# Optimization experiments

Measured on AMD Instinct MI355X. Metric: run time of the kernel, lower is better.

## Reference

```python
import jax, jax.numpy as jnp
import numpy as np

NV, NE, NI, D = 100000, 20000, 600000, 128

def setup_inputs() -> dict:
    key = jax.random.key(0)
    ks = jax.random.split(key, 16)
    inp = {
        'vfeat': jax.random.normal(ks[0], (NV, D), jnp.float32),
        'efeat': jax.random.normal(ks[1], (NE, D), jnp.float32),
        # positive regularization weights/sums (HNHN degree-based normalizers)
        'v_reg_weight': jax.random.uniform(ks[2], (NV, 1), jnp.float32, 0.5, 1.5),
        'v_reg_sum': jax.random.uniform(ks[3], (NV, 1), jnp.float32, 0.5, 1.5),
        'e_reg_weight': jax.random.uniform(ks[4], (NE, 1), jnp.float32, 0.5, 1.5),
        'e_reg_sum': jax.random.uniform(ks[5], (NE, 1), jnp.float32, 0.5, 1.5),
        'node_idx': jax.random.randint(ks[6], (NI,), 0, NV),
        'hedge_idx': jax.random.randint(ks[7], (NI,), 0, NE),
    }
    s = 1.0 / np.sqrt(D)
    inp['W1'] = jax.random.uniform(ks[8], (D, D), jnp.float32, -s, s)
    inp['b1'] = jax.random.uniform(ks[9], (D,), jnp.float32, -s, s)
    inp['Wve'] = jax.random.uniform(ks[10], (D, D), jnp.float32, -s, s)
    inp['bve'] = jax.random.uniform(ks[11], (D,), jnp.float32, -s, s)
    inp['Wev'] = jax.random.uniform(ks[12], (D, D), jnp.float32, -s, s)
    inp['bev'] = jax.random.uniform(ks[13], (D,), jnp.float32, -s, s)
    return inp


def reference(vfeat, efeat, v_reg_weight, v_reg_sum, e_reg_weight, e_reg_sum,
              node_idx, hedge_idx, W1, b1, Wve, bve, Wev, bev):
    # vertex projection (vtx_lin_1layer)
    feat_v = vfeat @ W1.T + b1                      # [NV, Dv]
    # node -> hyperedge pass ('in' etype)
    Wh_n = feat_v @ Wve.T + bve                     # [NV, De]
    w_in = v_reg_weight[node_idx] / e_reg_sum[hedge_idx]   # [NI, 1]
    feat_e = jax.ops.segment_sum(w_in * Wh_n[node_idx], hedge_idx,
                                 num_segments=NE)   # [NE, De]
    # hyperedge -> node pass ('con' etype)
    Wh_e = feat_e @ Wev.T + bev                     # [NE, Dv]
    w_con = e_reg_weight[hedge_idx] / v_reg_sum[node_idx]  # [NI, 1]
    feat_v_out = jax.ops.segment_sum(w_con * Wh_e[hedge_idx], node_idx,
                                     num_segments=NV)  # [NV, Dv]
    return feat_v_out
```

## Files before the change

kernel.cpp:

```cpp
#include <hip/hip_runtime.h>

#define D 128
#define PADE 16
#define PADV 4

typedef unsigned short ushort_t;
typedef short short8 __attribute__((ext_vector_type(8)));
typedef ushort_t ushort8v __attribute__((ext_vector_type(8)));
typedef float f32x4 __attribute__((ext_vector_type(4)));

static __device__ __forceinline__ unsigned short f2bf(float f){
  unsigned int b = __float_as_uint(f);
  unsigned int r = (b + 0x7FFFu + ((b >> 16) & 1u)) >> 16;
  return (unsigned short)r;
}
static __device__ __forceinline__ float bf2f(unsigned short u){
  return __uint_as_float(((unsigned int)u) << 16);
}


__global__ void k_u1(const float* __restrict__ W1, const float* __restrict__ Wve,
                     const float* __restrict__ b1, const float* __restrict__ bve,
                     float* __restrict__ Wcf, float* __restrict__ bc,
                     const float* __restrict__ vfeat, ushort_t* __restrict__ vbf, int nvd,
                     const int* __restrict__ node_idx, const int* __restrict__ hedge_idx, int ni,
                     int* __restrict__ cnt_e_pad, int* __restrict__ cnt_v_pad,
                     int* __restrict__ rank_e, int* __restrict__ rank_v,
                     int vb, int cb){
  int t = threadIdx.x;
  int i = blockIdx.x;
  if (i < 128){
    int r = i;
    if (t < D){
      float acc = 0.f;
      for (int k = 0; k < D; ++k) acc += Wve[r * D + k] * W1[k * D + t];
      Wcf[r * D + t] = acc;
      if (t == 0){
        float s = 0.f;
        for (int k = 0; k < D; ++k) s += Wve[r * D + k] * b1[k];
        bc[r] = s + bve[r];
      }
    }
    return;
  }
  int j = i - 128;
  int total = vb + cb;
  long a0 = (long)j * vb / total, a1 = (long)(j + 1) * vb / total;
  if (a1 != a0){
    size_t base = (size_t)a0 * 8192;
#pragma unroll
    for (int c = 0; c < 4; ++c){
      size_t e8 = base + (size_t)c * 2048 + (size_t)t * 8;
      if (e8 < (size_t)nvd){
        float4 v0 = *(const float4*)&vfeat[e8];
        float4 v1 = *(const float4*)&vfeat[e8 + 4];
        ushort8v h;
        h[0] = f2bf(v0.x); h[1] = f2bf(v0.y); h[2] = f2bf(v0.z); h[3] = f2bf(v0.w);
        h[4] = f2bf(v1.x); h[5] = f2bf(v1.y); h[6] = f2bf(v1.z); h[7] = f2bf(v1.w);
        *(ushort8v*)&vbf[e8] = h;
      }
    }
  } else {
    int idx = (int)(j - a0) * 256 + t;
    if (idx < ni){
      int n = node_idx[idx], h = hedge_idx[idx];
      rank_e[idx] = atomicAdd(&cnt_e_pad[h * PADE], 1);
      rank_v[idx] = atomicAdd(&cnt_v_pad[n * PADV], 1);
    }
  }
}


__device__ __forceinline__ void scan_partial_body(const int* cnt, int n, int stride,
                                                  int* bsum, int b){
  __shared__ int s[256];
  int t = threadIdx.x;
  int base = b * 1024;
  int acc = 0;
  for (int j = t; j < 1024; j += 256){
    int idx = base + j;
    if (idx < n) acc += cnt[(size_t)idx * stride];
  }
  s[t] = acc; __syncthreads();
  for (int o = 128; o > 0; o >>= 1){
    if (t < o) s[t] += s[t + o];
    __syncthreads();
  }
  if (t == 0) bsum[b] = s[0];
}

__global__ void k_scan_partial2(const int* __restrict__ ce, int ne, int* __restrict__ bse,
                                const int* __restrict__ cv, int nv, int* __restrict__ bsv,
                                int nbe){
  if ((int)blockIdx.x < nbe) scan_partial_body(ce, ne, PADE, bse, blockIdx.x);
  else                       scan_partial_body(cv, nv, PADV, bsv, blockIdx.x - nbe);
}

__device__ __forceinline__ void scan_final_body(const int* cnt, int n, int stride,
                                                const int* bsum, int nb,
                                                int* off, int* cout, int b){
  __shared__ int s[256];
  int t = threadIdx.x;
  int bv = (t < nb) ? bsum[t] : 0;
  s[t] = bv; __syncthreads();
  for (int o = 1; o < 256; o <<= 1){
    int x = (t >= o) ? s[t - o] : 0;
    __syncthreads();
    s[t] += x;
    __syncthreads();
  }
  int myb = (b == 0) ? 0 : s[b - 1];
  __syncthreads();

  int base = b * 1024 + t * 4;
  int v0 = (base + 0 < n) ? cnt[(size_t)(base + 0) * stride] : 0;
  int v1 = (base + 1 < n) ? cnt[(size_t)(base + 1) * stride] : 0;
  int v2 = (base + 2 < n) ? cnt[(size_t)(base + 2) * stride] : 0;
  int v3 = (base + 3 < n) ? cnt[(size_t)(base + 3) * stride] : 0;
  int lsum = v0 + v1 + v2 + v3;
  s[t] = lsum; __syncthreads();
  for (int o = 1; o < 256; o <<= 1){
    int x = (t >= o) ? s[t - o] : 0;
    __syncthreads();
    s[t] += x;
    __syncthreads();
  }
  int excl = s[t] - lsum + myb;
  if (base + 0 < n){ off[base + 0] = excl;                cout[base + 0] = v0; }
  if (base + 1 < n){ off[base + 1] = excl + v0;           cout[base + 1] = v1; }
  if (base + 2 < n){ off[base + 2] = excl + v0 + v1;      cout[base + 2] = v2; }
  if (base + 3 < n){ off[base + 3] = excl + v0 + v1 + v2; cout[base + 3] = v3; }
}

__global__ void k_scan_final2(const int* __restrict__ ce, int ne, const int* __restrict__ bse,
                              int* __restrict__ off_e, int* __restrict__ cnt_e,
                              const int* __restrict__ cv, int nv, const int* __restrict__ bsv,
                              int* __restrict__ off_v, int* __restrict__ cnt_v,
                              int nbe, int nbv){
  if ((int)blockIdx.x < nbe)
    scan_final_body(ce, ne, PADE, bse, nbe, off_e, cnt_e, blockIdx.x);
  else
    scan_final_body(cv, nv, PADV, bsv, nbv, off_v, cnt_v, blockIdx.x - nbe);
}


__global__ void k_u2(const float* __restrict__ Wev, const float* __restrict__ Wcf,
                     const float* __restrict__ bc,
                     ushort_t* __restrict__ Wcc, float* __restrict__ bvec1,
                     const int* __restrict__ node_idx, const int* __restrict__ hedge_idx,
                     const int* __restrict__ rank_e, int ni,
                     const int* __restrict__ off_e, int* __restrict__ elist_v){
  int t = threadIdx.x;
  int i = blockIdx.x;
  if (i < 128){
    int r = i;
    if (t < D){
      float acc = 0.f;
      for (int k = 0; k < D; ++k) acc += Wev[r * D + k] * Wcf[k * D + t];
      Wcc[r * D + t] = f2bf(acc);
      if (t == 0){
        float s = 0.f;
        for (int k = 0; k < D; ++k) s += Wev[r * D + k] * bc[k];
        bvec1[r] = s;
      }
    }
  } else {
    int idx = (i - 128) * 256 + t;
    if (idx < ni){
      int pe = off_e[hedge_idx[idx]] + rank_e[idx];
      elist_v[pe] = node_idx[idx];
    }
  }
}


__global__ void k_u3(const ushort_t* __restrict__ vbf,
                     const int* __restrict__ off_e, const int* __restrict__ cnt_e,
                     const int* __restrict__ elist,
                     const float* __restrict__ vrw, const float* __restrict__ ers,
                     float* __restrict__ agg, float* __restrict__ wsum,
                     int ne, int sb, int total,
                     const int* __restrict__ node_idx, const int* __restrict__ hedge_idx,
                     const int* __restrict__ rank_v, int ni,
                     const int* __restrict__ off_v, int* __restrict__ vlist_e){
  int i = blockIdx.x;
  long a0 = (long)i * sb / total, a1 = (long)(i + 1) * sb / total;
  if (a1 != a0){
    int tid = threadIdx.x;
    int seg = (int)a0 * 16 + (tid >> 4);
    if (seg >= ne) return;
    int l16 = tid & 15;
    int s = off_e[seg], n = cnt_e[seg];
    float inv = 1.0f / ers[seg];

    float acc[8];
#pragma unroll
    for (int c = 0; c < 8; ++c) acc[c] = 0.f;
    float wa = 0.f;

    int j = 0;
    for (; j + 2 <= n; j += 2){
      int r0 = elist[s + j];
      int r1 = elist[s + j + 1];
      float w0 = vrw[r0];
      float w1 = vrw[r1];
      ushort8v x0 = *(const ushort8v*)&vbf[(size_t)r0 * D + l16 * 8];
      ushort8v x1 = *(const ushort8v*)&vbf[(size_t)r1 * D + l16 * 8];
      wa += w0 + w1;
#pragma unroll
      for (int c = 0; c < 8; ++c) acc[c] += w0 * bf2f(x0[c]) + w1 * bf2f(x1[c]);
    }
    if (j < n){
      int r0 = elist[s + j];
      float w0 = vrw[r0];
      ushort8v x0 = *(const ushort8v*)&vbf[(size_t)r0 * D + l16 * 8];
      wa += w0;
#pragma unroll
      for (int c = 0; c < 8; ++c) acc[c] += w0 * bf2f(x0[c]);
    }

    float* dp = &agg[(size_t)seg * D + l16 * 8];
    float4 o0, o1;
    o0.x = acc[0] * inv; o0.y = acc[1] * inv; o0.z = acc[2] * inv; o0.w = acc[3] * inv;
    o1.x = acc[4] * inv; o1.y = acc[5] * inv; o1.z = acc[6] * inv; o1.w = acc[7] * inv;
    *(float4*)dp = o0;
    *(float4*)(dp + 4) = o1;
    if (l16 == 0) wsum[seg] = wa * inv;
  } else {
    int idx = (int)(i - a0) * 256 + threadIdx.x;
    if (idx < ni){
      int pv = off_v[node_idx[idx]] + rank_v[idx];
      vlist_e[pv] = hedge_idx[idx];
    }
  }
}


__global__ __launch_bounds__(256, 2)
void k_gemm_rs(const float* __restrict__ A, const ushort_t* __restrict__ Wb,
               const float* __restrict__ wsum, const float* __restrict__ bvec1,
               const float* __restrict__ bev, ushort_t* __restrict__ out, int M){
  __shared__ ushort_t Al[64 * D];

  const int t = threadIdx.x;
  const int w = t >> 6;
  const int l = t & 63;
  const int l15 = l & 15;
  const int lh = l >> 4;

  short8 breg[4][8];
#pragma unroll
  for (int kc = 0; kc < 4; ++kc)
#pragma unroll
    for (int n0 = 0; n0 < 8; ++n0)
      breg[kc][n0] = *(const short8*)&Wb[(n0 * 16 + l15) * D + kc * 32 + lh * 8];

  float bv1_r[8], bev_r[8];
#pragma unroll
  for (int n0 = 0; n0 < 8; ++n0){
    bv1_r[n0] = bvec1[n0 * 16 + l15];
    bev_r[n0] = bev[n0 * 16 + l15];
  }

  const int r_st = t >> 2;
  const int q_st = t & 3;
  const int ntile = (M + 63) >> 6;

  for (int tile = blockIdx.x; tile < ntile; tile += gridDim.x){
    const int row0 = tile << 6;
    __syncthreads();
    {
      int r = row0 + r_st;
      ushort8v h[4];
      if (r < M){
        const float4* src = (const float4*)&A[(size_t)r * D + q_st * 32];
        float4 v[8];
#pragma unroll
        for (int ii = 0; ii < 8; ++ii) v[ii] = src[ii];
#pragma unroll
        for (int c = 0; c < 4; ++c){
          h[c][0] = f2bf(v[2*c].x);   h[c][1] = f2bf(v[2*c].y);
          h[c][2] = f2bf(v[2*c].z);   h[c][3] = f2bf(v[2*c].w);
          h[c][4] = f2bf(v[2*c+1].x); h[c][5] = f2bf(v[2*c+1].y);
          h[c][6] = f2bf(v[2*c+1].z); h[c][7] = f2bf(v[2*c+1].w);
        }
      } else {
#pragma unroll
        for (int c = 0; c < 4; ++c) h[c] = (ushort8v){0,0,0,0,0,0,0,0};
      }
#pragma unroll
      for (int c = 0; c < 4; ++c){
        int col = q_st * 32 + c * 8;
        int swz = col ^ ((r_st & 7) << 3);
        *(ushort8v*)&Al[r_st * D + swz] = h[c];
      }
    }
    __syncthreads();

    f32x4 acc[8];
#pragma unroll
    for (int n0 = 0; n0 < 8; ++n0) acc[n0] = (f32x4){0.f, 0.f, 0.f, 0.f};

#pragma unroll
    for (int kc = 0; kc < 4; ++kc){
      const int arow = w * 16 + l15;
      const int acol = (kc * 32 + lh * 8) ^ ((l15 & 7) << 3);
      short8 a = *(const short8*)&Al[arow * D + acol];
#pragma unroll
      for (int n0 = 0; n0 < 8; ++n0)
        acc[n0] = __builtin_amdgcn_mfma_f32_16x16x32_bf16(a, breg[kc][n0], acc[n0], 0, 0, 0);
    }

    const int rbase = row0 + w * 16 + lh * 4;
    float w4[4];
#pragma unroll
    for (int rg = 0; rg < 4; ++rg)
      w4[rg] = (rbase + rg < M) ? wsum[rbase + rg] : 0.f;
#pragma unroll
    for (int n0 = 0; n0 < 8; ++n0){
      const int colo = n0 * 16 + l15;
#pragma unroll
      for (int rg = 0; rg < 4; ++rg){
        int row = rbase + rg;
        if (row < M)
          out[(size_t)row * D + colo] = f2bf(acc[n0][rg] + w4[rg] * bv1_r[n0] + bev_r[n0]);
      }
    }
  }
}


__global__ void k_scatter2(const ushort_t* __restrict__ src,
                           const int* __restrict__ off, const int* __restrict__ cnt,
                           const int* __restrict__ list,
                           const float* __restrict__ wnum, const float* __restrict__ dsum,
                           float* __restrict__ dst, int nseg){
  int tid = threadIdx.x;
  int seg = blockIdx.x * 16 + (tid >> 4);
  if (seg >= nseg) return;
  int l16 = tid & 15;
  int s = off[seg], n = cnt[seg];
  float inv = 1.0f / dsum[seg];

  float acc[8];
#pragma unroll
  for (int c = 0; c < 8; ++c) acc[c] = 0.f;

  int j = 0;
  for (; j + 2 <= n; j += 2){
    int r0 = list[s + j];
    int r1 = list[s + j + 1];
    float w0 = wnum[r0] * inv;
    float w1 = wnum[r1] * inv;
    ushort8v x0 = *(const ushort8v*)&src[(size_t)r0 * D + l16 * 8];
    ushort8v x1 = *(const ushort8v*)&src[(size_t)r1 * D + l16 * 8];
#pragma unroll
    for (int c = 0; c < 8; ++c) acc[c] += w0 * bf2f(x0[c]) + w1 * bf2f(x1[c]);
  }
  if (j < n){
    int r0 = list[s + j];
    float w0 = wnum[r0] * inv;
    ushort8v x0 = *(const ushort8v*)&src[(size_t)r0 * D + l16 * 8];
#pragma unroll
    for (int c = 0; c < 8; ++c) acc[c] += w0 * bf2f(x0[c]);
  }

  float* dp = &dst[(size_t)seg * D + l16 * 8];
  float4 o0, o1;
  o0.x = acc[0]; o0.y = acc[1]; o0.z = acc[2]; o0.w = acc[3];
  o1.x = acc[4]; o1.y = acc[5]; o1.z = acc[6]; o1.w = acc[7];
  *(float4*)dp = o0;
  *(float4*)(dp + 4) = o1;
}


static inline int cdiv(int a, int b){ return (a + b - 1) / b; }

extern "C" void kernel_launch(void* const* d_in, const int* in_sizes, int n_in,
                              void* d_out, int out_size, void* d_ws, size_t ws_size,
                              hipStream_t stream){
  const float* vfeat        = (const float*)d_in[0];
  const float* v_reg_weight = (const float*)d_in[2];
  const float* v_reg_sum    = (const float*)d_in[3];
  const float* e_reg_weight = (const float*)d_in[4];
  const float* e_reg_sum    = (const float*)d_in[5];
  const int*   node_idx     = (const int*)d_in[6];
  const int*   hedge_idx    = (const int*)d_in[7];
  const float* W1  = (const float*)d_in[8];
  const float* b1  = (const float*)d_in[9];
  const float* Wve = (const float*)d_in[10];
  const float* bve = (const float*)d_in[11];
  const float* Wev = (const float*)d_in[12];
  const float* bev = (const float*)d_in[13];

  const int NV = in_sizes[2];
  const int NE = in_sizes[4];
  const int NI = in_sizes[6];
  const int NVD = NV * D;

  char* p = (char*)d_ws;
  auto alloc = [&](size_t nbytes) -> void* {
    void* q = (void*)p;
    p += (nbytes + 255) & ~(size_t)255;
    return q;
  };

  char* zstart = p;
  int* cnt_e_pad = (int*)alloc((size_t)NE * PADE * 4);
  int* cnt_v_pad = (int*)alloc((size_t)NV * PADV * 4);
  size_t zbytes = (size_t)(p - zstart);

  int* cnt_e  = (int*)alloc((size_t)NE * 4);
  int* cnt_v  = (int*)alloc((size_t)NV * 4);
  int* off_e  = (int*)alloc((size_t)NE * 4);
  int* off_v  = (int*)alloc((size_t)NV * 4);
  int* bsum_e = (int*)alloc(1024 * 4);
  int* bsum_v = (int*)alloc(1024 * 4);
  int* rank_e = (int*)alloc((size_t)NI * 4);
  int* rank_v = (int*)alloc((size_t)NI * 4);
  int* elist_v = (int*)alloc((size_t)NI * 4);
  int* vlist_e = (int*)alloc((size_t)NI * 4);
  float* Wcf     = (float*)alloc((size_t)D * D * 4);
  float* bc      = (float*)alloc((size_t)D * 4);
  ushort_t* Wcc  = (ushort_t*)alloc((size_t)D * D * 2);
  float* bvec1   = (float*)alloc((size_t)D * 4);
  ushort_t* Wh_e = (ushort_t*)alloc((size_t)NE * D * 2);

  ushort_t* vbf  = (ushort_t*)d_out;
  float*    agg  = (float*)((char*)d_out + (size_t)NVD * 2);
  float*    wsum = (float*)((char*)d_out + (size_t)NVD * 2 + (size_t)NE * D * 4);

  hipMemsetAsync(zstart, 0, zbytes, stream);

  int cb = cdiv(NI, 256);
  int vb = cdiv(NVD, 8192);
  k_u1<<<128 + vb + cb, 256, 0, stream>>>(W1, Wve, b1, bve, Wcf, bc,
                                          vfeat, vbf, NVD,
                                          node_idx, hedge_idx, NI,
                                          cnt_e_pad, cnt_v_pad, rank_e, rank_v,
                                          vb, cb);

  int nbe = cdiv(NE, 1024), nbv = cdiv(NV, 1024);
  k_scan_partial2<<<nbe + nbv, 256, 0, stream>>>(cnt_e_pad, NE, bsum_e,
                                                 cnt_v_pad, NV, bsum_v, nbe);
  k_scan_final2<<<nbe + nbv, 256, 0, stream>>>(cnt_e_pad, NE, bsum_e, off_e, cnt_e,
                                               cnt_v_pad, NV, bsum_v, off_v, cnt_v,
                                               nbe, nbv);

  k_u2<<<128 + cb, 256, 0, stream>>>(Wev, Wcf, bc, Wcc, bvec1,
                                     node_idx, hedge_idx, rank_e, NI,
                                     off_e, elist_v);

  int sb = cdiv(NE, 16);
  int u3_total = sb + cb;
  k_u3<<<u3_total, 256, 0, stream>>>(vbf, off_e, cnt_e, elist_v,
                                     v_reg_weight, e_reg_sum,
                                     agg, wsum, NE, sb, u3_total,
                                     node_idx, hedge_idx, rank_v, NI,
                                     off_v, vlist_e);

  k_gemm_rs<<<cdiv(NE, 64), 256, 0, stream>>>(agg, Wcc, wsum, bvec1, bev, Wh_e, NE);

  k_scatter2<<<cdiv(NV, 16), 256, 0, stream>>>(Wh_e, off_v, cnt_v, vlist_e,
                                               e_reg_weight, v_reg_sum,
                                               (float*)d_out, NV);
}
```

Before: 166.0 us.

## Fuse hyperedge gather-aggregation with the Wev GEMM via shared memory

The hyperedge aggregation kernel now accumulates 64 hyperedges per block into a padded shared-memory tile and runs the bf16 MFMA projection directly from it, writing Wh_e. This removes the fp32 agg/wsum round trip through global memory and one kernel launch. In exchange each block does four times as many segments serially in the gather phase, holds about 34KB of LDS, and carries extra register pressure from the preloaded weight fragments, which can reduce occupancy and latency hiding for the irregular gathers.

```diff
diff --git a/kernel.cpp b/kernel.cpp
--- a/kernel.cpp
+++ b/kernel.cpp
@@ -3,6 +3,7 @@
 #define D 128
 #define PADE 16
 #define PADV 4
+#define AGLD 132
 
 typedef unsigned short ushort_t;
 typedef short short8 __attribute__((ext_vector_type(8)));
@@ -174,75 +175,79 @@
 }
 
 
-__global__ void k_u3(const ushort_t* __restrict__ vbf,
-                     const int* __restrict__ off_e, const int* __restrict__ cnt_e,
-                     const int* __restrict__ elist,
-                     const float* __restrict__ vrw, const float* __restrict__ ers,
-                     float* __restrict__ agg, float* __restrict__ wsum,
-                     int ne, int sb, int total,
-                     const int* __restrict__ node_idx, const int* __restrict__ hedge_idx,
-                     const int* __restrict__ rank_v, int ni,
-                     const int* __restrict__ off_v, int* __restrict__ vlist_e){
+__global__ __launch_bounds__(256, 2)
+void k_u3f(const ushort_t* __restrict__ vbf,
+           const int* __restrict__ off_e, const int* __restrict__ cnt_e,
+           const int* __restrict__ elist,
+           const float* __restrict__ vrw, const float* __restrict__ ers,
+           const ushort_t* __restrict__ Wcc, const float* __restrict__ bvec1,
+           const float* __restrict__ bev, ushort_t* __restrict__ Wh_e,
+           int ne, int sbf, int total,
+           const int* __restrict__ node_idx, const int* __restrict__ hedge_idx,
+           const int* __restrict__ rank_v, int ni,
+           const int* __restrict__ off_v, int* __restrict__ vlist_e){
+  __shared__ float aggl[64 * AGLD];
+  __shared__ float wsl[64];
+
   int i = blockIdx.x;
-  long a0 = (long)i * sb / total, a1 = (long)(i + 1) * sb / total;
-  if (a1 != a0){
-    int tid = threadIdx.x;
-    int seg = (int)a0 * 16 + (tid >> 4);
-    if (seg >= ne) return;
-    int l16 = tid & 15;
-    int s = off_e[seg], n = cnt_e[seg];
-    float inv = 1.0f / ers[seg];
-
-    float acc[8];
-#pragma unroll
-    for (int c = 0; c < 8; ++c) acc[c] = 0.f;
-    float wa = 0.f;
-
-    int j = 0;
-    for (; j + 2 <= n; j += 2){
-      int r0 = elist[s + j];
-      int r1 = elist[s + j + 1];
-      float w0 = vrw[r0];
-      float w1 = vrw[r1];
-      ushort8v x0 = *(const ushort8v*)&vbf[(size_t)r0 * D + l16 * 8];
-      ushort8v x1 = *(const ushort8v*)&vbf[(size_t)r1 * D + l16 * 8];
-      wa += w0 + w1;
-#pragma unroll
-      for (int c = 0; c < 8; ++c) acc[c] += w0 * bf2f(x0[c]) + w1 * bf2f(x1[c]);
-    }
-    if (j < n){
-      int r0 = elist[s + j];
-      float w0 = vrw[r0];
-      ushort8v x0 = *(const ushort8v*)&vbf[(size_t)r0 * D + l16 * 8];
-      wa += w0;
-#pragma unroll
-      for (int c = 0; c < 8; ++c) acc[c] += w0 * bf2f(x0[c]);
-    }
-
-    float* dp = &agg[(size_t)seg * D + l16 * 8];
-    float4 o0, o1;
-    o0.x = acc[0] * inv; o0.y = acc[1] * inv; o0.z = acc[2] * inv; o0.w = acc[3] * inv;
-    o1.x = acc[4] * inv; o1.y = acc[5] * inv; o1.z = acc[6] * inv; o1.w = acc[7] * inv;
-    *(float4*)dp = o0;
-    *(float4*)(dp + 4) = o1;
-    if (l16 == 0) wsum[seg] = wa * inv;
-  } else {
+  long a0 = (long)i * sbf / total, a1 = (long)(i + 1) * sbf / total;
+  if (a1 == a0){
     int idx = (int)(i - a0) * 256 + threadIdx.x;
     if (idx < ni){
       int pv = off_v[node_idx[idx]] + rank_v[idx];
       vlist_e[pv] = hedge_idx[idx];
     }
-  }
-}
-
-
-__global__ __launch_bounds__(256, 2)
-void k_gemm_rs(const float* __restrict__ A, const ushort_t* __restrict__ Wb,
-               const float* __restrict__ wsum, const float* __restrict__ bvec1,
-               const float* __restrict__ bev, ushort_t* __restrict__ out, int M){
-  __shared__ ushort_t Al[64 * D];
-
+    return;
+  }
+
+  const int blk = (int)a0;
   const int t = threadIdx.x;
+
+  {
+    int gid = t >> 4, l16 = t & 15;
+#pragma unroll
+    for (int it = 0; it < 4; ++it){
+      int row = it * 16 + gid;
+      int seg = blk * 64 + row;
+      float acc[8];
+#pragma unroll
+      for (int c = 0; c < 8; ++c) acc[c] = 0.f;
+      float wa = 0.f, inv = 0.f;
+      if (seg < ne){
+        int s = off_e[seg], n = cnt_e[seg];
+        inv = 1.0f / ers[seg];
+        int j = 0;
+        for (; j + 2 <= n; j += 2){
+          int r0 = elist[s + j];
+          int r1 = elist[s + j + 1];
+          float w0 = vrw[r0];
+          float w1 = vrw[r1];
+          ushort8v x0 = *(const ushort8v*)&vbf[(size_t)r0 * D + l16 * 8];
+          ushort8v x1 = *(const ushort8v*)&vbf[(size_t)r1 * D + l16 * 8];
+          wa += w0 + w1;
+#pragma unroll
+          for (int c = 0; c < 8; ++c) acc[c] += w0 * bf2f(x0[c]) + w1 * bf2f(x1[c]);
+        }
+        if (j < n){
+          int r0 = elist[s + j];
+          float w0 = vrw[r0];
+          ushort8v x0 = *(const ushort8v*)&vbf[(size_t)r0 * D + l16 * 8];
+          wa += w0;
+#pragma unroll
+          for (int c = 0; c < 8; ++c) acc[c] += w0 * bf2f(x0[c]);
+        }
+      }
+      float* ap = &aggl[row * AGLD + l16 * 8];
+      float4 o0, o1;
+      o0.x = acc[0] * inv; o0.y = acc[1] * inv; o0.z = acc[2] * inv; o0.w = acc[3] * inv;
+      o1.x = acc[4] * inv; o1.y = acc[5] * inv; o1.z = acc[6] * inv; o1.w = acc[7] * inv;
+      *(float4*)ap = o0;
+      *(float4*)(ap + 4) = o1;
+      if (l16 == 0) wsl[row] = wa * inv;
+    }
+  }
+  __syncthreads();
+
   const int w = t >> 6;
   const int l = t & 63;
   const int l15 = l & 15;
@@ -253,7 +258,7 @@
   for (int kc = 0; kc < 4; ++kc)
 #pragma unroll
     for (int n0 = 0; n0 < 8; ++n0)
-      breg[kc][n0] = *(const short8*)&Wb[(n0 * 16 + l15) * D + kc * 32 + lh * 8];
+      breg[kc][n0] = *(const short8*)&Wcc[(n0 * 16 + l15) * D + kc * 32 + lh * 8];
 
   float bv1_r[8], bev_r[8];
 #pragma unroll
@@ -262,69 +267,37 @@
     bev_r[n0] = bev[n0 * 16 + l15];
   }
 
-  const int r_st = t >> 2;
-  const int q_st = t & 3;
-  const int ntile = (M + 63) >> 6;
-
-  for (int tile = blockIdx.x; tile < ntile; tile += gridDim.x){
-    const int row0 = tile << 6;
-    __syncthreads();
-    {
-      int r = row0 + r_st;
-      ushort8v h[4];
-      if (r < M){
-        const float4* src = (const float4*)&A[(size_t)r * D + q_st * 32];
-        float4 v[8];
-#pragma unroll
-        for (int ii = 0; ii < 8; ++ii) v[ii] = src[ii];
-#pragma unroll
-        for (int c = 0; c < 4; ++c){
-          h[c][0] = f2bf(v[2*c].x);   h[c][1] = f2bf(v[2*c].y);
-          h[c][2] = f2bf(v[2*c].z);   h[c][3] = f2bf(v[2*c].w);
-          h[c][4] = f2bf(v[2*c+1].x); h[c][5] = f2bf(v[2*c+1].y);
-          h[c][6] = f2bf(v[2*c+1].z); h[c][7] = f2bf(v[2*c+1].w);
-        }
-      } else {
-#pragma unroll
-        for (int c = 0; c < 4; ++c) h[c] = (ushort8v){0,0,0,0,0,0,0,0};
-      }
-#pragma unroll
-      for (int c = 0; c < 4; ++c){
-        int col = q_st * 32 + c * 8;
-        int swz = col ^ ((r_st & 7) << 3);
-        *(ushort8v*)&Al[r_st * D + swz] = h[c];
-      }
-    }
-    __syncthreads();
-
-    f32x4 acc[8];
-#pragma unroll
-    for (int n0 = 0; n0 < 8; ++n0) acc[n0] = (f32x4){0.f, 0.f, 0.f, 0.f};
-
-#pragma unroll
-    for (int kc = 0; kc < 4; ++kc){
-      const int arow = w * 16 + l15;
-      const int acol = (kc * 32 + lh * 8) ^ ((l15 & 7) << 3);
-      short8 a = *(const short8*)&Al[arow * D + acol];
-#pragma unroll
-      for (int n0 = 0; n0 < 8; ++n0)
-        acc[n0] = __builtin_amdgcn_mfma_f32_16x16x32_bf16(a, breg[kc][n0], acc[n0], 0, 0, 0);
-    }
-
-    const int rbase = row0 + w * 16 + lh * 4;
-    float w4[4];
-#pragma unroll
-    for (int rg = 0; rg < 4; ++rg)
-      w4[rg] = (rbase + rg < M) ? wsum[rbase + rg] : 0.f;
-#pragma unroll
-    for (int n0 = 0; n0 < 8; ++n0){
-      const int colo = n0 * 16 + l15;
-#pragma unroll
-      for (int rg = 0; rg < 4; ++rg){
-        int row = rbase + rg;
-        if (row < M)
-          out[(size_t)row * D + colo] = f2bf(acc[n0][rg] + w4[rg] * bv1_r[n0] + bev_r[n0]);
-      }
+  f32x4 acc2[8];
+#pragma unroll
+  for (int n0 = 0; n0 < 8; ++n0) acc2[n0] = (f32x4){0.f, 0.f, 0.f, 0.f};
+
+#pragma unroll
+  for (int kc = 0; kc < 4; ++kc){
+    const float* ap = &aggl[(w * 16 + l15) * AGLD + kc * 32 + lh * 8];
+    float4 va = *(const float4*)ap;
+    float4 vb = *(const float4*)(ap + 4);
+    short8 af;
+    af[0] = (short)f2bf(va.x); af[1] = (short)f2bf(va.y);
+    af[2] = (short)f2bf(va.z); af[3] = (short)f2bf(va.w);
+    af[4] = (short)f2bf(vb.x); af[5] = (short)f2bf(vb.y);
+    af[6] = (short)f2bf(vb.z); af[7] = (short)f2bf(vb.w);
+#pragma unroll
+    for (int n0 = 0; n0 < 8; ++n0)
+      acc2[n0] = __builtin_amdgcn_mfma_f32_16x16x32_bf16(af, breg[kc][n0], acc2[n0], 0, 0, 0);
+  }
+
+  const int lrow0 = w * 16 + lh * 4;
+  float w4[4];
+#pragma unroll
+  for (int rg = 0; rg < 4; ++rg) w4[rg] = wsl[lrow0 + rg];
+#pragma unroll
+  for (int n0 = 0; n0 < 8; ++n0){
+    const int colo = n0 * 16 + l15;
+#pragma unroll
+    for (int rg = 0; rg < 4; ++rg){
+      int row = blk * 64 + lrow0 + rg;
+      if (row < ne)
+        Wh_e[(size_t)row * D + colo] = f2bf(acc2[n0][rg] + w4[rg] * bv1_r[n0] + bev_r[n0]);
     }
   }
 }
@@ -427,8 +400,6 @@
   ushort_t* Wh_e = (ushort_t*)alloc((size_t)NE * D * 2);
 
   ushort_t* vbf  = (ushort_t*)d_out;
-  float*    agg  = (float*)((char*)d_out + (size_t)NVD * 2);
-  float*    wsum = (float*)((char*)d_out + (size_t)NVD * 2 + (size_t)NE * D * 4);
 
   hipMemsetAsync(zstart, 0, zbytes, stream);
 
@@ -451,15 +422,14 @@
                                      node_idx, hedge_idx, rank_e, NI,
                                      off_e, elist_v);
 
-  int sb = cdiv(NE, 16);
-  int u3_total = sb + cb;
-  k_u3<<<u3_total, 256, 0, stream>>>(vbf, off_e, cnt_e, elist_v,
-                                     v_reg_weight, e_reg_sum,
-                                     agg, wsum, NE, sb, u3_total,
-                                     node_idx, hedge_idx, rank_v, NI,
-                                     off_v, vlist_e);
-
-  k_gemm_rs<<<cdiv(NE, 64), 256, 0, stream>>>(agg, Wcc, wsum, bvec1, bev, Wh_e, NE);
+  int sbf = cdiv(NE, 64);
+  int u3_total = sbf + cb;
+  k_u3f<<<u3_total, 256, 0, stream>>>(vbf, off_e, cnt_e, elist_v,
+                                      v_reg_weight, e_reg_sum,
+                                      Wcc, bvec1, bev, Wh_e,
+                                      NE, sbf, u3_total,
+                                      node_idx, hedge_idx, rank_v, NI,
+                                      off_v, vlist_e);
 
   k_scatter2<<<cdiv(NV, 16), 256, 0, stream>>>(Wh_e, off_v, cnt_v, vlist_e,
                                                e_reg_weight, v_reg_sum,
```

After: 193.7 us. 16.7% more time.
